# Performance work log

Measured on AMD Instinct MI355X. Metric: run time of the kernel, lower is better.

## Reference

```python
import jax, jax.numpy as jnp
import numpy as np

NUM_HEADS = 16
EPS = 1e-6
ROPE_THETA = 10000.0


def _rmsnorm_fp32(x, w):
    # RMSNorm computed in fp32, scale by learned weight (per head_dim)
    xf = x.astype(jnp.float32)
    var = jnp.mean(xf * xf, axis=-1, keepdims=True)
    return (xf * jax.lax.rsqrt(var + EPS) * w.astype(jnp.float32)).astype(x.dtype)


def _rope_3d_angles(T, H, W, head_dim):
    # split head_dim across (t,h,w) axes; all parts even
    dh = 2 * ((head_dim // 3) // 2)
    dw = dh
    dt = head_dim - dh - dw

    def axis_ang(L, d):
        inv = 1.0 / (ROPE_THETA ** (jnp.arange(0, d, 2, dtype=jnp.float32) / d))
        return jnp.arange(L, dtype=jnp.float32)[:, None] * inv[None, :]  # [L, d//2]

    at = axis_ang(T, dt)  # [T, dt/2]
    ah = axis_ang(H, dh)  # [H, dh/2]
    aw = axis_ang(W, dw)  # [W, dw/2]
    # broadcast to [T,H,W, head_dim//2] then flatten to [N, head_dim//2]
    at_g = jnp.broadcast_to(at[:, None, None, :], (T, H, W, dt // 2))
    ah_g = jnp.broadcast_to(ah[None, :, None, :], (T, H, W, dh // 2))
    aw_g = jnp.broadcast_to(aw[None, None, :, :], (T, H, W, dw // 2))
    ang = jnp.concatenate([at_g, ah_g, aw_g], axis=-1).reshape(T * H * W, head_dim // 2)
    return jnp.cos(ang), jnp.sin(ang)


def _apply_rope(x, cos, sin):
    # x: [B,Hh,N,D]; cos/sin: [N, D/2]; interleaved complex-pair rotation
    xr = x[..., 0::2]
    xi = x[..., 1::2]
    c = cos[None, None, :, :]
    s = sin[None, None, :, :]
    out_r = xr * c - xi * s
    out_i = xr * s + xi * c
    return jnp.stack([out_r, out_i], axis=-1).reshape(x.shape)


def setup_inputs() -> dict:
    key = jax.random.key(0)
    ks = jax.random.split(key, 7)
    dim, hd = 2048, 128
    x = jax.random.normal(ks[0], (1, 2048, dim), dtype=jnp.float32)
    qkv_w = jax.random.normal(ks[1], (3 * dim, dim), dtype=jnp.float32) * (dim ** -0.5)
    qkv_b = jax.random.normal(ks[2], (3 * dim,), dtype=jnp.float32) * 0.02
    proj_w = jax.random.normal(ks[3], (dim, dim), dtype=jnp.float32) * (dim ** -0.5)
    proj_b = jax.random.normal(ks[4], (dim,), dtype=jnp.float32) * 0.02
    q_norm_w = jnp.ones((hd,), dtype=jnp.float32)
    k_norm_w = jnp.ones((hd,), dtype=jnp.float32)
    return {"x": x, "qkv_w": qkv_w, "qkv_b": qkv_b, "proj_w": proj_w,
            "proj_b": proj_b, "q_norm_w": q_norm_w, "k_norm_w": k_norm_w,
            "t_dim": 8, "h_dim": 16, "w_dim": 16}


def reference(x, qkv_w, qkv_b, proj_w, proj_b, q_norm_w, k_norm_w, t_dim, h_dim, w_dim):
    B, N, C = x.shape
    Hh = NUM_HEADS
    D = C // Hh
    scale = D ** -0.5
    # QKV projection (torch Linear: x @ W.T + b)
    qkv = x @ qkv_w.T + qkv_b                      # [B,N,3C]
    qkv = qkv.reshape(B, N, 3, Hh, D).transpose(2, 0, 3, 1, 4)  # [3,B,Hh,N,D]
    q, k, v = qkv[0], qkv[1], qkv[2]
    q = _rmsnorm_fp32(q, q_norm_w)
    k = _rmsnorm_fp32(k, k_norm_w)
    cos, sin = _rope_3d_angles(t_dim, h_dim, w_dim, D)
    q = _apply_rope(q, cos, sin)
    k = _apply_rope(k, cos, sin)
    # SDPA (non-causal)
    scores = jnp.einsum('bhqd,bhkd->bhqk', q, k) * scale
    attn = jax.nn.softmax(scores, axis=-1)
    out = jnp.einsum('bhqk,bhkd->bhqd', attn, v)   # [B,Hh,N,D]
    out = out.transpose(0, 2, 1, 3).reshape(B, N, C)
    return out @ proj_w.T + proj_b
```

## Files before the change

kernel.cpp:

```cpp
#include <hip/hip_runtime.h>
#include <hip/hip_bf16.h>
#include <cstdint>
#include <cstddef>

typedef __attribute__((ext_vector_type(8))) short bf16x8;
typedef __attribute__((ext_vector_type(4))) float f32x4;
typedef __attribute__((ext_vector_type(16))) float f32x16;

#define AS1 __attribute__((address_space(1)))
#define AS3 __attribute__((address_space(3)))

__device__ __forceinline__ void gload_lds16(const void* g, void* l) {
  __builtin_amdgcn_global_load_lds((const AS1 void*)g, (AS3 void*)l, 16, 0, 0);
}

__device__ __forceinline__ unsigned short f2bf(float x) {
  __hip_bfloat16 h = __float2bfloat16(x);
  return __builtin_bit_cast(unsigned short, h);
}
__device__ __forceinline__ float bf2f(unsigned short u) {
  return __builtin_bit_cast(float, (unsigned int)u << 16);
}
__device__ __forceinline__ unsigned cvtpk(float a, float b) {
  unsigned r;
  asm("v_cvt_pk_bf16_f32 %0, %1, %2" : "=v"(r) : "v"(a), "v"(b));
  return r;
}
__device__ __forceinline__ void pswap(unsigned& x, unsigned& y) {
  asm volatile("v_permlane32_swap_b32 %0, %1" : "+v"(x), "+v"(y));
}

__global__ __launch_bounds__(256) void k_cvt3(const float* __restrict__ a, unsigned short* __restrict__ ao, int na4,
                                              const float* __restrict__ b, unsigned short* __restrict__ bo, int nb4,
                                              const float* __restrict__ c, unsigned short* __restrict__ co, int nc4,
                                              float* __restrict__ cosT, float* __restrict__ sinT,
                                              const int* __restrict__ hdim, const int* __restrict__ wdim) {
  const int stride = gridDim.x * 256;
  for (int i = blockIdx.x * 256 + threadIdx.x; i < na4; i += stride) {
    float4 v = reinterpret_cast<const float4*>(a)[i];
    ushort4 o; o.x = f2bf(v.x); o.y = f2bf(v.y); o.z = f2bf(v.z); o.w = f2bf(v.w);
    reinterpret_cast<ushort4*>(ao)[i] = o;
  }
  for (int i = blockIdx.x * 256 + threadIdx.x; i < nb4; i += stride) {
    float4 v = reinterpret_cast<const float4*>(b)[i];
    ushort4 o; o.x = f2bf(v.x); o.y = f2bf(v.y); o.z = f2bf(v.z); o.w = f2bf(v.w);
    reinterpret_cast<ushort4*>(bo)[i] = o;
  }
  for (int i = blockIdx.x * 256 + threadIdx.x; i < nc4; i += stride) {
    float4 v = reinterpret_cast<const float4*>(c)[i];
    ushort4 o; o.x = f2bf(v.x); o.y = f2bf(v.y); o.z = f2bf(v.z); o.w = f2bf(v.w);
    reinterpret_cast<ushort4*>(co)[i] = o;
  }
  const int H = *hdim, W = *wdim;
  for (int idx = blockIdx.x * 256 + threadIdx.x; idx < 2048 * 64; idx += stride) {
    const int n = idx >> 6, j = idx & 63;
    const int w = n % W;
    const int rem = n / W;
    const int h = rem % H;
    const int t = rem / H;
    float pos, i2, d;
    if (j < 22)      { pos = (float)t; i2 = (float)(2 * j);        d = 44.f; }
    else if (j < 43) { pos = (float)h; i2 = (float)(2 * (j - 22)); d = 42.f; }
    else             { pos = (float)w; i2 = (float)(2 * (j - 43)); d = 42.f; }
    const float ang = pos * powf(10000.0f, -i2 / d);
    cosT[idx] = cosf(ang);
    sinT[idx] = sinf(ang);
  }
}

__global__ __launch_bounds__(256, 2) void k_gemmQKV(const unsigned short* __restrict__ A,
                                                    const unsigned short* __restrict__ B,
                                                    const float* __restrict__ bias,
                                                    unsigned short* __restrict__ C,
                                                    int M, int N, int K) {
  __shared__ __align__(16) char lds[81920];
  const int tid = threadIdx.x;
  const int lane = tid & 63;
  const int wid = tid >> 6;
  const int wr = wid >> 1, wc = wid & 1;

  const int xcd = blockIdx.x & 7;
  const int t0 = blockIdx.x >> 3;
  const int bx = xcd * 4 + (t0 & 3);
  const int by = t0 >> 2;
  const int row0 = by * 128, col0 = bx * 192;
  const int NT = K >> 5;

  auto stageA = [&](int kcol0, char* slot) {
#pragma unroll
    for (int r = 0; r < 2; ++r) {
      const int off = r * 4096 + tid * 16;
      const int pair = off >> 7;
      const int un = (off & 127) ^ ((pair & 7) << 4);
      const int grow = pair * 2 + (un >> 6);
      gload_lds16(A + (size_t)(row0 + grow) * K + kcol0 + ((un & 63) >> 1),
                  slot + r * 4096 + wid * 1024);
    }
  };
  auto stageB = [&](int kcol0, char* slot) {
#pragma unroll
    for (int r = 0; r < 3; ++r) {
      const int off = r * 4096 + tid * 16;
      const int pair = off >> 7;
      const int un = (off & 127) ^ ((pair & 7) << 4);
      const int grow = pair * 2 + (un >> 6);
      gload_lds16(B + (size_t)(col0 + grow) * K + kcol0 + ((un & 63) >> 1),
                  slot + r * 4096 + wid * 1024);
    }
  };
  auto frag = [&](const char* slot, int r, int kb) -> bf16x8 {
    return *reinterpret_cast<const bf16x8*>(
        slot + (r >> 1) * 128 + ((((r & 1) << 6) + kb) ^ (((r >> 1) & 7) << 4)));
  };

  f32x4 acc[4][6];
#pragma unroll
  for (int i = 0; i < 4; ++i)
#pragma unroll
    for (int j = 0; j < 6; ++j) acc[i][j] = (f32x4){0.f, 0.f, 0.f, 0.f};

#pragma unroll
  for (int p = 0; p < 3; ++p) {
    stageA(p * 32, lds + p * 8192);
    stageB(p * 32, lds + 32768 + p * 12288);
  }
  asm volatile("s_waitcnt vmcnt(10)" ::: "memory");
  __builtin_amdgcn_s_barrier();

  const int kb = (lane >> 4) << 4;
  for (int j = 0; j < NT; ++j) {
    const char* baseA = lds + (j & 3) * 8192;
    const char* baseB = lds + 32768 + (j & 3) * 12288;
    bf16x8 af[4], bq[6];
#pragma unroll
    for (int fr = 0; fr < 4; ++fr) af[fr] = frag(baseA, wr * 64 + fr * 16 + (lane & 15), kb);
#pragma unroll
    for (int fc = 0; fc < 6; ++fc) bq[fc] = frag(baseB, wc * 96 + fc * 16 + (lane & 15), kb);

    const int jp = j + 3;
    if (jp < NT) {
      stageA(jp * 32, lds + (jp & 3) * 8192);
      stageB(jp * 32, lds + 32768 + (jp & 3) * 12288);
      asm volatile("s_waitcnt vmcnt(10)" ::: "memory");
    } else if (j + 2 < NT) {
      asm volatile("s_waitcnt vmcnt(5)" ::: "memory");
    } else if (j + 1 < NT) {
      asm volatile("s_waitcnt vmcnt(0)" ::: "memory");
    }
    if (j + 1 < NT) __builtin_amdgcn_s_barrier();

    __builtin_amdgcn_s_setprio(1);
#pragma unroll
    for (int fr = 0; fr < 4; ++fr)
#pragma unroll
      for (int fc = 0; fc < 6; ++fc)
        acc[fr][fc] = __builtin_amdgcn_mfma_f32_16x16x32_bf16(af[fr], bq[fc], acc[fr][fc], 0, 0, 0);
    __builtin_amdgcn_s_setprio(0);
  }

#pragma unroll
  for (int fr = 0; fr < 4; ++fr)
#pragma unroll
    for (int fc = 0; fc < 6; ++fc) {
      const int col = col0 + wc * 96 + fc * 16 + (lane & 15);
      const float bv = bias[col];
#pragma unroll
      for (int jj = 0; jj < 4; ++jj) {
        const int row = row0 + wr * 64 + fr * 16 + (lane >> 4) * 4 + jj;
        C[(size_t)row * N + col] = f2bf(acc[fr][fc][jj] + bv);
      }
    }
}

__global__ __launch_bounds__(256, 2) void k_gemmProj(const unsigned short* __restrict__ A,
                                                     const unsigned short* __restrict__ B,
                                                     const float* __restrict__ bias,
                                                     float* __restrict__ out,
                                                     int M, int N, int K) {
  __shared__ __align__(16) char lds[49152];
  const int tid = threadIdx.x;
  const int lane = tid & 63;
  const int wid = tid >> 6;
  const int wr = wid >> 1, wc = wid & 1;
  const int row0 = blockIdx.y * 64;
  const int col0 = blockIdx.x * 128;
  const int NT = K >> 5;

  auto stageA = [&](int kcol0, char* slot) {
    const int off = tid * 16;
    const int pair = off >> 7;
    const int un = (off & 127) ^ ((pair & 7) << 4);
    const int grow = pair * 2 + (un >> 6);
    gload_lds16(A + (size_t)(row0 + grow) * K + kcol0 + ((un & 63) >> 1),
                slot + wid * 1024);
  };
  auto stageB = [&](int kcol0, char* slot) {
#pragma unroll
    for (int r = 0; r < 2; ++r) {
      const int off = r * 4096 + tid * 16;
      const int pair = off >> 7;
      const int un = (off & 127) ^ ((pair & 7) << 4);
      const int grow = pair * 2 + (un >> 6);
      gload_lds16(B + (size_t)(col0 + grow) * K + kcol0 + ((un & 63) >> 1),
                  slot + r * 4096 + wid * 1024);
    }
  };
  auto frag = [&](const char* slot, int r, int kb) -> bf16x8 {
    return *reinterpret_cast<const bf16x8*>(
        slot + (r >> 1) * 128 + ((((r & 1) << 6) + kb) ^ (((r >> 1) & 7) << 4)));
  };

  f32x4 acc[2][4];
#pragma unroll
  for (int i = 0; i < 2; ++i)
#pragma unroll
    for (int j = 0; j < 4; ++j) acc[i][j] = (f32x4){0.f, 0.f, 0.f, 0.f};

#pragma unroll
  for (int p = 0; p < 3; ++p) {
    stageA(p * 32, lds + p * 4096);
    stageB(p * 32, lds + 16384 + p * 8192);
  }
  asm volatile("s_waitcnt vmcnt(6)" ::: "memory");
  __builtin_amdgcn_s_barrier();

  const int kb = (lane >> 4) << 4;
  for (int j = 0; j < NT; ++j) {
    const char* baseA = lds + (j & 3) * 4096;
    const char* baseB = lds + 16384 + (j & 3) * 8192;
    bf16x8 af[2], bq[4];
#pragma unroll
    for (int fr = 0; fr < 2; ++fr) af[fr] = frag(baseA, wr * 32 + fr * 16 + (lane & 15), kb);
#pragma unroll
    for (int fc = 0; fc < 4; ++fc) bq[fc] = frag(baseB, wc * 64 + fc * 16 + (lane & 15), kb);

    const int jp = j + 3;
    if (jp < NT) {
      stageA(jp * 32, lds + (jp & 3) * 4096);
      stageB(jp * 32, lds + 16384 + (jp & 3) * 8192);
      asm volatile("s_waitcnt vmcnt(6)" ::: "memory");
    } else if (j + 2 < NT) {
      asm volatile("s_waitcnt vmcnt(3)" ::: "memory");
    } else if (j + 1 < NT) {
      asm volatile("s_waitcnt vmcnt(0)" ::: "memory");
    }
    if (j + 1 < NT) __builtin_amdgcn_s_barrier();

    __builtin_amdgcn_s_setprio(1);
#pragma unroll
    for (int fr = 0; fr < 2; ++fr)
#pragma unroll
      for (int fc = 0; fc < 4; ++fc)
        acc[fr][fc] = __builtin_amdgcn_mfma_f32_16x16x32_bf16(af[fr], bq[fc], acc[fr][fc], 0, 0, 0);
    __builtin_amdgcn_s_setprio(0);
  }

#pragma unroll
  for (int fr = 0; fr < 2; ++fr)
#pragma unroll
    for (int fc = 0; fc < 4; ++fc) {
      const int col = col0 + wc * 64 + fc * 16 + (lane & 15);
      const float bv = bias[col];
#pragma unroll
      for (int jj = 0; jj < 4; ++jj) {
        const int row = row0 + wr * 32 + fr * 16 + (lane >> 4) * 4 + jj;
        out[(size_t)row * N + col] = acc[fr][fc][jj] + bv;
      }
    }
}

__global__ __launch_bounds__(256) void k_post(const unsigned short* __restrict__ qkv,
                                              const float* __restrict__ qw,
                                              const float* __restrict__ kw,
                                              const float* __restrict__ cosT,
                                              const float* __restrict__ sinT,
                                              unsigned short* __restrict__ qo,
                                              unsigned short* __restrict__ ko,
                                              unsigned short* __restrict__ vt2) {
  __shared__ __align__(16) unsigned short tile[64][136];
  if (blockIdx.x < 8192) {
    const int lane = threadIdx.x & 63;
    const int wid = threadIdx.x >> 6;
    const int pair = blockIdx.x * 4 + wid;
    const int n = pair >> 4, h = pair & 15;
    const float c = cosT[n * 64 + lane];
    const float s = sinT[n * 64 + lane];
#pragma unroll
    for (int sq = 0; sq < 2; ++sq) {
      const unsigned short* src = qkv + (size_t)n * 6144 + sq * 2048 + h * 128;
      const unsigned int vp = reinterpret_cast<const unsigned int*>(src)[lane];
      const float vx = bf2f((unsigned short)(vp & 0xffff));
      const float vy = bf2f((unsigned short)(vp >> 16));
      float ss = vx * vx + vy * vy;
#pragma unroll
      for (int m = 1; m < 64; m <<= 1) ss += __shfl_xor(ss, m, 64);
      const float r = rsqrtf(ss * (1.0f / 128.0f) + 1e-6f);
      float2 wv = reinterpret_cast<const float2*>(sq == 0 ? qw : kw)[lane];
      const float xr = vx * r * wv.x;
      const float xi = vy * r * wv.y;
      float orr = xr * c - xi * s;
      float oi  = xr * s + xi * c;
      if (sq == 0) { orr *= 0.08838834764831845f; oi *= 0.08838834764831845f; }
      unsigned short* dst = (sq == 0 ? qo : ko) + ((size_t)h * 2048 + n) * 128 + 2 * lane;
      const unsigned int pk = (unsigned int)f2bf(orr) | ((unsigned int)f2bf(oi) << 16);
      *reinterpret_cast<unsigned int*>(dst) = pk;
    }
  } else {
    const int idx = blockIdx.x - 8192;
    const int h = idx >> 5;
    const int n0 = (idx & 31) * 64;
    const int t = threadIdx.x;
    {
      const int row = t >> 2;
      const int c0 = (t & 3) * 32;
      const unsigned short* src = qkv + (size_t)(n0 + row) * 6144 + 4096 + h * 128 + c0;
#pragma unroll
      for (int j = 0; j < 32; j += 8)
        *reinterpret_cast<bf16x8*>(&tile[row][c0 + j]) =
            *reinterpret_cast<const bf16x8*>(src + j);
    }
    __syncthreads();
#pragma unroll
    for (int g4 = 0; g4 < 4; ++g4) {
      const int g = g4 * 256 + t;
      const int c = g >> 8;
      const int dblk = (g >> 6) & 3;
      const int p = g & 63;
      const int d = dblk * 32 + (p & 31);
      const int hi = p >> 5;
      bf16x8 o;
#pragma unroll
      for (int e = 0; e < 8; ++e) o[e] = (short)tile[c * 16 + hi * 8 + e][d];
      const size_t oidx = ((((size_t)h * 128 + (n0 >> 4) + c) * 4 + dblk) * 64 + p) * 8;
      *reinterpret_cast<bf16x8*>(vt2 + oidx) = o;
    }
  }
}

__global__ __launch_bounds__(256) void k_fattn(const unsigned short* __restrict__ q,
                                               const unsigned short* __restrict__ k,
                                               const unsigned short* __restrict__ vt2,
                                               unsigned short* __restrict__ Onorm,
                                               float* __restrict__ lseb) {
  __shared__ __align__(16) unsigned short Ks[2][64 * 128];
  __shared__ __align__(16) unsigned short Vs[2][64 * 128];
  const int lane = threadIdx.x & 63;
  const int wid = threadIdx.x >> 6;
  const int hi2 = lane >> 5;
  const int ql = lane & 31;
  const int bid = blockIdx.x;
  const int h = bid & 15;
  const int qb = (bid >> 4) & 15;
  const int ksp = bid >> 8;
  const int q0 = qb * 128 + wid * 32;
  const int kbase = ksp * 1024;

  auto stageK = [&](int buf, int kt2) {
#pragma unroll
    for (int r = 0; r < 4; ++r) {
      const int off = r * 4096 + (wid * 64 + lane) * 16;
      const int row = off >> 8;
      const int colb = (off & 255) ^ ((row & 15) << 4);
      gload_lds16(k + ((size_t)h * 2048 + kbase + kt2 * 64 + row) * 128 + (colb >> 1),
                  (char*)Ks[buf] + r * 4096 + wid * 1024);
    }
  };
  auto stageV = [&](int buf, int kt2) {
    const unsigned short* vbase = vt2 + ((size_t)h * 128 + (kbase >> 4) + kt2 * 4) * 2048;
#pragma unroll
    for (int r = 0; r < 4; ++r)
      gload_lds16(vbase + r * 2048 + (wid * 64 + lane) * 8,
                  (char*)Vs[buf] + r * 4096 + wid * 1024);
  };

  bf16x8 qf[8];
  {
    const unsigned short* qp = q + ((size_t)h * 2048 + q0 + ql) * 128 + hi2 * 8;
#pragma unroll
    for (int c = 0; c < 8; ++c) qf[c] = *reinterpret_cast<const bf16x8*>(qp + c * 16);
  }
  f32x16 O[4];
#pragma unroll
  for (int i = 0; i < 4; ++i)
#pragma unroll
    for (int j = 0; j < 16; ++j) O[i][j] = 0.f;
  float m = -1e30f, l = 0.f;

  stageK(0, 0);
  stageV(0, 0);
  asm volatile("s_waitcnt vmcnt(0)" ::: "memory");
  __builtin_amdgcn_s_barrier();

  const int kswz = (lane & 15) << 4;
  for (int kt = 0; kt < 16; ++kt) {
    const int cur = kt & 1;
    const bool pf = (kt + 1 < 16);
    if (pf) { stageK(cur ^ 1, kt + 1); stageV(cur ^ 1, kt + 1); }

    f32x16 s0, s1;
#pragma unroll
    for (int j = 0; j < 16; ++j) { s0[j] = 0.f; s1[j] = 0.f; }
    __builtin_amdgcn_s_setprio(1);
#pragma unroll
    for (int c = 0; c < 8; ++c) {
      bf16x8 a0 = *reinterpret_cast<const bf16x8*>(
          (const char*)Ks[cur] + ql * 256 + ((c * 32 + hi2 * 16) ^ kswz));
      s0 = __builtin_amdgcn_mfma_f32_32x32x16_bf16(a0, qf[c], s0, 0, 0, 0);
    }
#pragma unroll
    for (int c = 0; c < 8; ++c) {
      bf16x8 a1 = *reinterpret_cast<const bf16x8*>(
          (const char*)Ks[cur] + (32 + ql) * 256 + ((c * 32 + hi2 * 16) ^ kswz));
      s1 = __builtin_amdgcn_mfma_f32_32x32x16_bf16(a1, qf[c], s1, 0, 0, 0);
    }
    __builtin_amdgcn_s_setprio(0);

    float mt = s0[0];
#pragma unroll
    for (int j = 1; j < 16; ++j) mt = fmaxf(mt, s0[j]);
#pragma unroll
    for (int j = 0; j < 16; ++j) mt = fmaxf(mt, s1[j]);
    mt = fmaxf(mt, __shfl_xor(mt, 32, 64));

    if (!__all(mt <= m + 8.0f)) {
      const float mn = fmaxf(m, mt);
      const float al = __expf(m - mn);
      m = mn;
      l *= al;
#pragma unroll
      for (int i = 0; i < 4; ++i)
#pragma unroll
        for (int j = 0; j < 16; ++j) O[i][j] *= al;
    }
    float rs = 0.f;
#pragma unroll
    for (int j = 0; j < 16; ++j) {
      s0[j] = __expf(s0[j] - m); rs += s0[j];
      s1[j] = __expf(s1[j] - m); rs += s1[j];
    }
    rs += __shfl_xor(rs, 32, 64);
    l += rs;

    bf16x8 pfr[4];
#pragma unroll
    for (int half = 0; half < 2; ++half) {
      const f32x16& sv = half ? s1 : s0;
      unsigned a[8];
#pragma unroll
      for (int j2 = 0; j2 < 8; ++j2) a[j2] = cvtpk(sv[2 * j2], sv[2 * j2 + 1]);
      pswap(a[0], a[2]);
      pswap(a[1], a[3]);
      pswap(a[4], a[6]);
      pswap(a[5], a[7]);
      union { uint4 u; bf16x8 v; } p0, p1;
      p0.u.x = a[0]; p0.u.y = a[1]; p0.u.z = a[2]; p0.u.w = a[3];
      p1.u.x = a[4]; p1.u.y = a[5]; p1.u.z = a[6]; p1.u.w = a[7];
      pfr[half * 2 + 0] = p0.v;
      pfr[half * 2 + 1] = p1.v;
    }

    __builtin_amdgcn_s_setprio(1);
#pragma unroll
    for (int dblk = 0; dblk < 4; ++dblk) {
#pragma unroll
      for (int c2 = 0; c2 < 4; ++c2) {
        bf16x8 va = *reinterpret_cast<const bf16x8*>(
            (const char*)Vs[cur] + ((c2 * 4 + dblk) * 64 + lane) * 16);
        O[dblk] = __builtin_amdgcn_mfma_f32_32x32x16_bf16(va, pfr[c2], O[dblk], 0, 0, 0);
      }
    }
    __builtin_amdgcn_s_setprio(0);

    if (pf) {
      asm volatile("s_waitcnt vmcnt(0)" ::: "memory");
      __builtin_amdgcn_s_barrier();
    }
  }

  const float rl = 1.0f / l;
  const int n = q0 + ql;
  unsigned short* ob = Onorm + (((size_t)(ksp * 16 + h) * 2048) + n) * 128;
#pragma unroll
  for (int dblk = 0; dblk < 4; ++dblk)
#pragma unroll
    for (int a = 0; a < 4; ++a) {
      uint2 w;
      w.x = (unsigned)f2bf(O[dblk][a * 4 + 0] * rl) | ((unsigned)f2bf(O[dblk][a * 4 + 1] * rl) << 16);
      w.y = (unsigned)f2bf(O[dblk][a * 4 + 2] * rl) | ((unsigned)f2bf(O[dblk][a * 4 + 3] * rl) << 16);
      *reinterpret_cast<uint2*>(ob + dblk * 32 + a * 8 + hi2 * 4) = w;
    }
  if (hi2 == 0)
    lseb[(size_t)(ksp * 16 + h) * 2048 + n] = m + logf(l);
}

__global__ __launch_bounds__(256) void k_merge(const unsigned short* __restrict__ Onorm,
                                               const float* __restrict__ lseb,
                                               unsigned short* __restrict__ att) {
  const int idx = blockIdx.x * 256 + threadIdx.x;
  const int n = idx >> 8;
  const int r = idx & 255;
  const int h = r >> 4;
  const int d0 = (r & 15) * 8;
  const float l0 = lseb[(size_t)h * 2048 + n];
  const float l1 = lseb[(size_t)(16 + h) * 2048 + n];
  const float M = fmaxf(l0, l1);
  float w0 = __expf(l0 - M), w1 = __expf(l1 - M);
  const float inv = 1.0f / (w0 + w1);
  w0 *= inv; w1 *= inv;
  const bf16x8 o0 = *reinterpret_cast<const bf16x8*>(
      Onorm + ((size_t)h * 2048 + n) * 128 + d0);
  const bf16x8 o1 = *reinterpret_cast<const bf16x8*>(
      Onorm + ((size_t)(16 + h) * 2048 + n) * 128 + d0);
  bf16x8 o;
#pragma unroll
  for (int e = 0; e < 8; ++e)
    o[e] = (short)f2bf(bf2f((unsigned short)o0[e]) * w0 + bf2f((unsigned short)o1[e]) * w1);
  *reinterpret_cast<bf16x8*>(att + (size_t)n * 2048 + h * 128 + d0) = o;
}

extern "C" void kernel_launch(void* const* d_in, const int* in_sizes, int n_in,
                              void* d_out, int out_size, void* d_ws, size_t ws_size,
                              hipStream_t stream) {
  (void)in_sizes; (void)n_in; (void)out_size; (void)ws_size;
  const float* x      = (const float*)d_in[0];
  const float* qkv_w  = (const float*)d_in[1];
  const float* qkv_b  = (const float*)d_in[2];
  const float* proj_w = (const float*)d_in[3];
  const float* proj_b = (const float*)d_in[4];
  const float* q_nw   = (const float*)d_in[5];
  const float* k_nw   = (const float*)d_in[6];
  const int* h_dim    = (const int*)d_in[8];
  const int* w_dim    = (const int*)d_in[9];
  float* out = (float*)d_out;

  char* ws = (char*)d_ws;
  size_t off = 0;
  auto carve = [&](size_t bytes) -> void* {
    void* p = ws + off;
    off += (bytes + 255) & ~(size_t)255;
    return p;
  };
  unsigned short* x_bf   = (unsigned short*)carve(2048ull * 2048 * 2);
  unsigned short* w1_bf  = (unsigned short*)carve(6144ull * 2048 * 2);
  unsigned short* w2_bf  = (unsigned short*)carve(2048ull * 2048 * 2);
  unsigned short* qkvb   = (unsigned short*)carve(2048ull * 6144 * 2);
  unsigned short* q_bf   = (unsigned short*)carve(16ull * 2048 * 128 * 2);
  unsigned short* k_bf   = (unsigned short*)carve(16ull * 2048 * 128 * 2);
  unsigned short* vt2_bf = (unsigned short*)carve(16ull * 2048 * 128 * 2);
  unsigned short* att_bf = (unsigned short*)carve(2048ull * 2048 * 2);
  unsigned short* on_bf  = (unsigned short*)carve(2ull * 16 * 2048 * 128 * 2);
  float*          lseb   = (float*)carve(2ull * 16 * 2048 * 4);
  float*          cosT   = (float*)carve(2048ull * 64 * 4);
  float*          sinT   = (float*)carve(2048ull * 64 * 4);

  hipLaunchKernelGGL(k_cvt3, dim3(2048), dim3(256), 0, stream,
                     x, x_bf, 2048 * 2048 / 4,
                     qkv_w, w1_bf, 6144 * 2048 / 4,
                     proj_w, w2_bf, 2048 * 2048 / 4,
                     cosT, sinT, h_dim, w_dim);
  hipLaunchKernelGGL(k_gemmQKV, dim3(512), dim3(256), 0, stream,
                     x_bf, w1_bf, qkv_b, qkvb, 2048, 6144, 2048);
  hipLaunchKernelGGL(k_post, dim3(8704), dim3(256), 0, stream,
                     qkvb, q_nw, k_nw, cosT, sinT, q_bf, k_bf, vt2_bf);
  hipLaunchKernelGGL(k_fattn, dim3(512), dim3(256), 0, stream,
                     q_bf, k_bf, vt2_bf, on_bf, lseb);
  hipLaunchKernelGGL(k_merge, dim3(2048), dim3(256), 0, stream, on_bf, lseb, att_bf);
  hipLaunchKernelGGL(k_gemmProj, dim3(16, 32), dim3(256), 0, stream,
                     att_bf, w2_bf, proj_b, out, 2048, 2048, 2048);
}
```

Baseline: 166.4 us.

## Rewrite QKV GEMM with 256x256 tiles, 8 waves and quadrant-interleaved prefetch

Replaces the 128x192-tile, 256-thread QKV GEMM with a 256x256-tile, 512-thread kernel using 64-wide K steps and a double-buffered 128KB LDS. Each K step is split into four MFMA quadrants separated by barriers. The A and B prefetch loads for step j+2 are issued between quadrants so memory traffic overlaps compute. Larger tiles raise operand reuse and cut global and LDS traffic per flop. The cost is only 192 blocks, fewer than the CU count, plus extra barriers and the register pressure of a large accumulator.

Measured after the change: 174.1 us. +4.6%, slower.

```diff
diff --git a/kernel.cpp b/kernel.cpp
--- a/kernel.cpp
+++ b/kernel.cpp
@@ -68,44 +68,33 @@
   }
 }
 
-__global__ __launch_bounds__(256, 2) void k_gemmQKV(const unsigned short* __restrict__ A,
-                                                    const unsigned short* __restrict__ B,
-                                                    const float* __restrict__ bias,
-                                                    unsigned short* __restrict__ C,
-                                                    int M, int N, int K) {
-  __shared__ __align__(16) char lds[81920];
+__global__ __launch_bounds__(512, 2) void k_gemmQKV8(const unsigned short* __restrict__ A,
+                                                     const unsigned short* __restrict__ B,
+                                                     const float* __restrict__ bias,
+                                                     unsigned short* __restrict__ C,
+                                                     int M, int N, int K) {
+  __shared__ __align__(16) char lds[131072];
   const int tid = threadIdx.x;
   const int lane = tid & 63;
   const int wid = tid >> 6;
-  const int wr = wid >> 1, wc = wid & 1;
+  const int wr = wid >> 2, wc = wid & 3;
 
   const int xcd = blockIdx.x & 7;
   const int t0 = blockIdx.x >> 3;
-  const int bx = xcd * 4 + (t0 & 3);
-  const int by = t0 >> 2;
-  const int row0 = by * 128, col0 = bx * 192;
-  const int NT = K >> 5;
-
-  auto stageA = [&](int kcol0, char* slot) {
+  const int bx = xcd * 3 + t0 % 3;
+  const int by = t0 / 3;
+  const int row0 = by * 256, col0 = bx * 256;
+  const int NT = K >> 6;
+
+  auto stage_slot = [&](const unsigned short* src, int grow0, int kcol0, char* slot) {
 #pragma unroll
     for (int r = 0; r < 2; ++r) {
-      const int off = r * 4096 + tid * 16;
+      const int off = r * 8192 + tid * 16;
       const int pair = off >> 7;
       const int un = (off & 127) ^ ((pair & 7) << 4);
       const int grow = pair * 2 + (un >> 6);
-      gload_lds16(A + (size_t)(row0 + grow) * K + kcol0 + ((un & 63) >> 1),
-                  slot + r * 4096 + wid * 1024);
-    }
-  };
-  auto stageB = [&](int kcol0, char* slot) {
-#pragma unroll
-    for (int r = 0; r < 3; ++r) {
-      const int off = r * 4096 + tid * 16;
-      const int pair = off >> 7;
-      const int un = (off & 127) ^ ((pair & 7) << 4);
-      const int grow = pair * 2 + (un >> 6);
-      gload_lds16(B + (size_t)(col0 + grow) * K + kcol0 + ((un & 63) >> 1),
-                  slot + r * 4096 + wid * 1024);
+      gload_lds16(src + (size_t)(grow0 + grow) * K + kcol0 + ((un & 63) >> 1),
+                  slot + r * 8192 + wid * 1024);
     }
   };
   auto frag = [&](const char* slot, int r, int kb) -> bf16x8 {
@@ -113,61 +102,125 @@
         slot + (r >> 1) * 128 + ((((r & 1) << 6) + kb) ^ (((r >> 1) & 7) << 4)));
   };
 
-  f32x4 acc[4][6];
-#pragma unroll
-  for (int i = 0; i < 4; ++i)
-#pragma unroll
-    for (int j = 0; j < 6; ++j) acc[i][j] = (f32x4){0.f, 0.f, 0.f, 0.f};
-
-#pragma unroll
-  for (int p = 0; p < 3; ++p) {
-    stageA(p * 32, lds + p * 8192);
-    stageB(p * 32, lds + 32768 + p * 12288);
-  }
-  asm volatile("s_waitcnt vmcnt(10)" ::: "memory");
+  f32x4 acc[8][4];
+#pragma unroll
+  for (int i = 0; i < 8; ++i)
+#pragma unroll
+    for (int j = 0; j < 4; ++j) acc[i][j] = (f32x4){0.f, 0.f, 0.f, 0.f};
+
+#pragma unroll
+  for (int p = 0; p < 2; ++p) {
+    char* buf = lds + p * 65536;
+    stage_slot(A, row0, p * 64,      buf);
+    stage_slot(A, row0, p * 64 + 32, buf + 16384);
+    stage_slot(B, col0, p * 64,      buf + 32768);
+    stage_slot(B, col0, p * 64 + 32, buf + 49152);
+  }
+  asm volatile("s_waitcnt vmcnt(8)" ::: "memory");
   __builtin_amdgcn_s_barrier();
 
   const int kb = (lane >> 4) << 4;
+  bf16x8 ar[2][4][2];
+  bf16x8 br[2][2][2];
+
   for (int j = 0; j < NT; ++j) {
-    const char* baseA = lds + (j & 3) * 8192;
-    const char* baseB = lds + 32768 + (j & 3) * 12288;
-    bf16x8 af[4], bq[6];
-#pragma unroll
-    for (int fr = 0; fr < 4; ++fr) af[fr] = frag(baseA, wr * 64 + fr * 16 + (lane & 15), kb);
-#pragma unroll
-    for (int fc = 0; fc < 6; ++fc) bq[fc] = frag(baseB, wc * 96 + fc * 16 + (lane & 15), kb);
-
-    const int jp = j + 3;
-    if (jp < NT) {
-      stageA(jp * 32, lds + (jp & 3) * 8192);
-      stageB(jp * 32, lds + 32768 + (jp & 3) * 12288);
-      asm volatile("s_waitcnt vmcnt(10)" ::: "memory");
-    } else if (j + 2 < NT) {
-      asm volatile("s_waitcnt vmcnt(5)" ::: "memory");
+    const char* buf = lds + (j & 1) * 65536;
+    char* pbuf = lds + (j & 1) * 65536;
+    const bool pf = (j + 2 < NT);
+    const int kn = (j + 2) * 64;
+
+#pragma unroll
+    for (int fi = 0; fi < 4; ++fi)
+#pragma unroll
+      for (int ks = 0; ks < 2; ++ks)
+        ar[0][fi][ks] = frag(buf + ks * 16384, wr * 128 + fi * 16 + (lane & 15), kb);
+#pragma unroll
+    for (int fj = 0; fj < 2; ++fj)
+#pragma unroll
+      for (int ks = 0; ks < 2; ++ks)
+        br[0][fj][ks] = frag(buf + 32768 + ks * 16384, wc * 64 + fj * 16 + (lane & 15), kb);
+    __builtin_amdgcn_s_barrier();
+    asm volatile("s_waitcnt lgkmcnt(0)" ::: "memory");
+    __builtin_amdgcn_s_setprio(1);
+#pragma unroll
+    for (int fi = 0; fi < 4; ++fi)
+#pragma unroll
+      for (int fj = 0; fj < 2; ++fj)
+#pragma unroll
+        for (int ks = 0; ks < 2; ++ks)
+          acc[fi][fj] = __builtin_amdgcn_mfma_f32_16x16x32_bf16(ar[0][fi][ks], br[0][fj][ks], acc[fi][fj], 0, 0, 0);
+    __builtin_amdgcn_s_setprio(0);
+    __builtin_amdgcn_s_barrier();
+
+#pragma unroll
+    for (int fi = 0; fi < 4; ++fi)
+#pragma unroll
+      for (int ks = 0; ks < 2; ++ks)
+        ar[1][fi][ks] = frag(buf + ks * 16384, wr * 128 + (fi + 4) * 16 + (lane & 15), kb);
+#pragma unroll
+    for (int fj = 0; fj < 2; ++fj)
+#pragma unroll
+      for (int ks = 0; ks < 2; ++ks)
+        br[1][fj][ks] = frag(buf + 32768 + ks * 16384, wc * 64 + (fj + 2) * 16 + (lane & 15), kb);
+    __builtin_amdgcn_s_barrier();
+    asm volatile("s_waitcnt lgkmcnt(0)" ::: "memory");
+    __builtin_amdgcn_s_setprio(1);
+#pragma unroll
+    for (int fi = 0; fi < 4; ++fi)
+#pragma unroll
+      for (int fj = 0; fj < 2; ++fj)
+#pragma unroll
+        for (int ks = 0; ks < 2; ++ks)
+          acc[fi + 4][fj + 2] = __builtin_amdgcn_mfma_f32_16x16x32_bf16(ar[1][fi][ks], br[1][fj][ks], acc[fi + 4][fj + 2], 0, 0, 0);
+    __builtin_amdgcn_s_setprio(0);
+    __builtin_amdgcn_s_barrier();
+
+    if (pf) {
+      stage_slot(A, row0, kn,      pbuf);
+      stage_slot(A, row0, kn + 32, pbuf + 16384);
+    }
+    __builtin_amdgcn_s_barrier();
+    __builtin_amdgcn_s_setprio(1);
+#pragma unroll
+    for (int fi = 0; fi < 4; ++fi)
+#pragma unroll
+      for (int fj = 0; fj < 2; ++fj)
+#pragma unroll
+        for (int ks = 0; ks < 2; ++ks)
+          acc[fi][fj + 2] = __builtin_amdgcn_mfma_f32_16x16x32_bf16(ar[0][fi][ks], br[1][fj][ks], acc[fi][fj + 2], 0, 0, 0);
+    __builtin_amdgcn_s_setprio(0);
+    __builtin_amdgcn_s_barrier();
+
+    if (pf) {
+      stage_slot(B, col0, kn,      pbuf + 32768);
+      stage_slot(B, col0, kn + 32, pbuf + 49152);
+      asm volatile("s_waitcnt vmcnt(8)" ::: "memory");
     } else if (j + 1 < NT) {
       asm volatile("s_waitcnt vmcnt(0)" ::: "memory");
     }
-    if (j + 1 < NT) __builtin_amdgcn_s_barrier();
-
+    __builtin_amdgcn_s_barrier();
     __builtin_amdgcn_s_setprio(1);
 #pragma unroll
-    for (int fr = 0; fr < 4; ++fr)
-#pragma unroll
-      for (int fc = 0; fc < 6; ++fc)
-        acc[fr][fc] = __builtin_amdgcn_mfma_f32_16x16x32_bf16(af[fr], bq[fc], acc[fr][fc], 0, 0, 0);
+    for (int fi = 0; fi < 4; ++fi)
+#pragma unroll
+      for (int fj = 0; fj < 2; ++fj)
+#pragma unroll
+        for (int ks = 0; ks < 2; ++ks)
+          acc[fi + 4][fj] = __builtin_amdgcn_mfma_f32_16x16x32_bf16(ar[1][fi][ks], br[0][fj][ks], acc[fi + 4][fj], 0, 0, 0);
     __builtin_amdgcn_s_setprio(0);
-  }
-
-#pragma unroll
-  for (int fr = 0; fr < 4; ++fr)
-#pragma unroll
-    for (int fc = 0; fc < 6; ++fc) {
-      const int col = col0 + wc * 96 + fc * 16 + (lane & 15);
+    __builtin_amdgcn_s_barrier();
+  }
+
+#pragma unroll
+  for (int fi = 0; fi < 8; ++fi)
+#pragma unroll
+    for (int fj = 0; fj < 4; ++fj) {
+      const int col = col0 + wc * 64 + fj * 16 + (lane & 15);
       const float bv = bias[col];
 #pragma unroll
       for (int jj = 0; jj < 4; ++jj) {
-        const int row = row0 + wr * 64 + fr * 16 + (lane >> 4) * 4 + jj;
-        C[(size_t)row * N + col] = f2bf(acc[fr][fc][jj] + bv);
+        const int row = row0 + wr * 128 + fi * 16 + (lane >> 4) * 4 + jj;
+        C[(size_t)row * N + col] = f2bf(acc[fi][fj][jj] + bv);
       }
     }
 }
@@ -558,7 +611,7 @@
                      qkv_w, w1_bf, 6144 * 2048 / 4,
                      proj_w, w2_bf, 2048 * 2048 / 4,
                      cosT, sinT, h_dim, w_dim);
-  hipLaunchKernelGGL(k_gemmQKV, dim3(512), dim3(256), 0, stream,
+  hipLaunchKernelGGL(k_gemmQKV8, dim3(192), dim3(512), 0, stream,
                      x_bf, w1_bf, qkv_b, qkvb, 2048, 6144, 2048);
   hipLaunchKernelGGL(k_post, dim3(8704), dim3(256), 0, stream,
                      qkvb, q_nw, k_nw, cosT, sinT, q_bf, k_bf, vt2_bf);
```
